# Performance work log

Hardware: AMD Instinct MI355X
Metric: run time of the kernel (lower is better)

The kernel has to match this reference:

```python
import jax, jax.numpy as jnp
import numpy as np

EPS = 1e-12
B, C, H, M, E, P = 2, 20000, 64, 8, 200000, 3


def setup_inputs() -> dict:
    key = jax.random.key(0)
    ks = jax.random.split(key, 24)
    inp = {}
    inp["features"] = jax.random.normal(ks[0], (B, C, H), jnp.float32)
    inp["positions"] = jax.random.normal(ks[1], (B, C, P), jnp.float32)
    inp["edge_index"] = jax.random.randint(ks[2], (2, E), 0, C)
    inp["degree"] = jax.random.randint(ks[3], (C,), 1, 33).astype(jnp.float32)
    inp["cell_node_indices"] = jax.random.randint(ks[4], (C, M), 0, C)
    mask = (jax.random.uniform(ks[5], (C, M)) > 0.3).astype(jnp.float32)
    inp["cell_node_mask"] = mask.at[:, 0].set(1.0)  # first node always valid (pad semantics)

    def lin(k, fan_in, fan_out):
        return (jax.random.normal(k, (fan_in, fan_out), jnp.float32) / np.sqrt(fan_in)).astype(jnp.float32)

    # message MLP: Linear(2H+4 -> H), SiLU, Linear(H -> H)
    inp["W1"] = lin(ks[6], 2 * H + 4, H); inp["b1"] = jnp.zeros((H,), jnp.float32)
    inp["W2"] = lin(ks[7], H, H);         inp["b2"] = jnp.zeros((H,), jnp.float32)
    # position MLP: Linear(H -> H), SiLU, Linear(H -> 1)
    inp["P1"] = lin(ks[8], H, H);  inp["pb1"] = jnp.zeros((H,), jnp.float32)
    inp["P2"] = lin(ks[9], H, 1);  inp["pb2"] = jnp.zeros((1,), jnp.float32)
    # update MLP: Linear(2H -> H), SiLU, Linear(H -> H)
    inp["U1"] = lin(ks[10], 2 * H, H); inp["ub1"] = jnp.zeros((H,), jnp.float32)
    inp["U2"] = lin(ks[11], H, H);     inp["ub2"] = jnp.zeros((H,), jnp.float32)
    return inp


def _mlp(x, Wa, ba, Wb, bb):
    return jax.nn.silu(x @ Wa + ba) @ Wb + bb


def _forward(features, positions, edge_index, degree, cell_node_indices, cell_node_mask,
             W1, b1, W2, b2, P1, pb1, P2, pb2, U1, ub1, U2, ub2):
    src, dst = edge_index[0], edge_index[1]
    # gather padded node positions per cell: [B, C, M, P]
    node_pos = positions[:, cell_node_indices]

    h_src = features[:, src]                      # [B,E,H]
    h_dst = features[:, dst]
    rel = positions[:, src] - positions[:, dst]   # [B,E,P]
    dist = jnp.linalg.norm(rel, axis=-1, keepdims=True)  # [B,E,1]

    sp = node_pos[:, src]                         # [B,E,M,P]
    dp = node_pos[:, dst]
    mx = cell_node_mask[src]                      # [E,M]
    my = cell_node_mask[dst]

    # pairwise distances [B,E,M,M] via gram trick (avoids [B,E,M,M,P] intermediate)
    sp2 = jnp.sum(sp * sp, -1)                    # [B,E,M]
    dp2 = jnp.sum(dp * dp, -1)
    cross = jnp.einsum('bemp,benp->bemn', sp, dp)
    d = jnp.sqrt(jnp.maximum(sp2[..., :, None] + dp2[..., None, :] - 2.0 * cross, 0.0) + EPS)

    # masked pairwise-distance sum
    w = mx[:, :, None] * my[:, None, :]           # [E,M,M]
    pairwise = jnp.sum(d * w[None], axis=(-1, -2))  # [B,E]

    # centroid distance
    denx = jnp.maximum(mx.sum(-1, keepdims=True), EPS)  # [E,1]
    deny = jnp.maximum(my.sum(-1, keepdims=True), EPS)
    cx = jnp.sum(sp * mx[None, :, :, None], axis=2) / denx[None]  # [B,E,P]
    cy = jnp.sum(dp * my[None, :, :, None], axis=2) / deny[None]
    centroid = jnp.linalg.norm(cx - cy, axis=-1)  # [B,E]

    # Hausdorff distance (masked min/max)
    inf = jnp.float32(jnp.inf)
    d_xy = jnp.where(my[None, :, None, :] <= 0, inf, d)
    min_xy = jnp.where(mx[None] <= 0, 0.0, d_xy.min(-1))  # [B,E,M]
    h_xy = min_xy.max(-1)                                  # [B,E]
    d_yx = jnp.where(mx[None, :, None, :] <= 0, inf, jnp.swapaxes(d, -1, -2))
    min_yx = jnp.where(my[None] <= 0, 0.0, d_yx.min(-1))
    h_yx = min_yx.max(-1)
    haus = jnp.maximum(h_xy, h_yx)

    invariants = jnp.concatenate([dist, pairwise[..., None], centroid[..., None], haus[..., None]], -1)  # [B,E,4]
    msg_in = jnp.concatenate([h_src, h_dst, invariants], -1)  # [B,E,2H+4]
    messages = _mlp(msg_in, W1, b1, W2, b2)                   # [B,E,H]

    # scatter-aggregate into destination cells, degree-normalize
    agg = jnp.zeros_like(features).at[:, dst].add(messages)
    agg = agg / jnp.maximum(degree, 1.0)[None, :, None]

    # position update
    wts = jnp.tanh(_mlp(messages, P1, pb1, P2, pb2))          # [B,E,1]
    pos_upd = jnp.zeros_like(positions).at[:, dst].add(wts * rel)

    new_features = features + _mlp(jnp.concatenate([features, agg], -1), U1, ub1, U2, ub2)
    new_positions = positions + pos_upd
    return new_features, new_positions


def reference(features, positions, edge_index, degree, cell_node_indices, cell_node_mask,
              W1, b1, W2, b2, P1, pb1, P2, pb2, U1, ub1, U2, ub2):
    return _forward(features, positions, edge_index, degree, cell_node_indices, cell_node_mask,
                    W1, b1, W2, b2, P1, pb1, P2, pb2, U1, ub1, U2, ub2)
```

## Files before the change

### kernel.cpp

```cpp
#include <hip/hip_runtime.h>
#include <hip/hip_bf16.h>

#define B_ 2
#define C_ 20000
#define H_ 64
#define M_ 8
#define E_ 200000
#define P_ 3
#define EPS_ 1e-12f
#define ET_ (E_ / 64)

typedef __attribute__((ext_vector_type(8))) short short8;
typedef __attribute__((ext_vector_type(4))) float float4v;

__device__ __forceinline__ float rcp_(float x)  { return __builtin_amdgcn_rcpf(x); }
__device__ __forceinline__ float sqrt_(float x) { return __builtin_amdgcn_sqrtf(x); }
__device__ __forceinline__ float silu_(float x) {
    return x * __builtin_amdgcn_rcpf(1.f + __expf(-x));
}
__device__ __forceinline__ float tanh_(float x) {
    float e = __expf(2.f * x);
    return 1.f - 2.f * __builtin_amdgcn_rcpf(e + 1.f);
}
__device__ __forceinline__ unsigned short f2b(float f) {
    unsigned u = __float_as_uint(f);
    unsigned r = (u + 0x7FFF + ((u >> 16) & 1)) >> 16;
    return (unsigned short)r;
}
__device__ __forceinline__ float b2f(unsigned short h) {
    return __uint_as_float(((unsigned)h) << 16);
}
__device__ __forceinline__ unsigned pk2u(float a, float b) {
    __hip_bfloat162 h = __float22bfloat162_rn(make_float2(a, b));
    unsigned u; __builtin_memcpy(&u, &h, sizeof(u)); return u;
}
__device__ __forceinline__ float lo16f(unsigned u) { return __uint_as_float(u << 16); }
__device__ __forceinline__ float hi16f(unsigned u) { return __uint_as_float(u & 0xFFFF0000u); }

#define W1S_OFF 0
#define W2S_OFF 8192
#define P1S_OFF 12288
#define U1S_OFF 16384
#define U2S_OFF 24576
#define WBUF_ELEMS 28672

#define NB_PREP  120
#define NB_FEATB 2500
#define NB_DESC  157
#define NB_HIST  782
#define NB_ZAGG  2500
#define NB_PCOPY 118
#define NB_COMBO (NB_PREP + NB_FEATB + NB_DESC + NB_HIST + NB_ZAGG + NB_PCOPY)


__global__ __launch_bounds__(256) void combo_kernel(
    const float* __restrict__ W1, const float* __restrict__ W2,
    const float* __restrict__ P1, const float* __restrict__ U1,
    const float* __restrict__ U2, unsigned short* __restrict__ wbuf,
    const float* __restrict__ feat, unsigned short* __restrict__ featb,
    const float* __restrict__ pos, const int* __restrict__ cni,
    const float* __restrict__ mask, unsigned* __restrict__ descp,
    const int* __restrict__ ei, int* __restrict__ cnt,
    float* __restrict__ aggf, float* __restrict__ out_pos)
{
    const int bid = blockIdx.x;
    if (bid < NB_PREP) {
        int t = bid * 256 + threadIdx.x;
        if (t >= WBUF_ELEMS) return;
        const float* W; int e;
        if (t < W2S_OFF)      { W = W1; e = t; }
        else if (t < U1S_OFF) { W = (t < P1S_OFF) ? W2 : P1; e = (t < P1S_OFF) ? t - W2S_OFF : t - P1S_OFF; }
        else if (t < U2S_OFF) { W = U1; e = t - U1S_OFF; }
        else                  { W = U2; e = t - U2S_OFF; }
        int j = e & 7, lane = (e >> 3) & 63, nt = (e >> 9) & 3, kk = e >> 11;
        int k = kk * 32 + ((lane >> 4) * 8) + j;
        int n = nt * 16 + (lane & 15);
        wbuf[t] = f2b(W[k * 64 + n]);
    } else if (bid < NB_PREP + NB_FEATB) {
        int t = (bid - NB_PREP) * 256 + threadIdx.x;
        float4 v = *(const float4*)&feat[(size_t)t * 4];
        *(uint2*)&featb[(size_t)t * 4] = make_uint2(pk2u(v.x, v.y), pk2u(v.z, v.w));
    } else if (bid < NB_PREP + NB_FEATB + NB_DESC) {
        int tid = (bid - NB_PREP - NB_FEATB) * 256 + threadIdx.x;
        if (tid >= B_ * C_) return;
        int b = tid / C_, c = tid - b * C_;
        const float* pb = pos + (size_t)b * C_ * P_;
        unsigned* D = descp + (size_t)tid * 32;
        int4 n0 = *(const int4*)&cni[c*8];
        int4 n1 = *(const int4*)&cni[c*8 + 4];
        float4 m0 = *(const float4*)&mask[c*8];
        float4 m1 = *(const float4*)&mask[c*8 + 4];
        int ni[8] = {n0.x, n0.y, n0.z, n0.w, n1.x, n1.y, n1.z, n1.w};
        float mm[8] = {m0.x, m0.y, m0.z, m0.w, m1.x, m1.y, m1.z, m1.w};
        float sx = 0.f, sy = 0.f, sz = 0.f, sm = 0.f;
        #pragma unroll
        for (int m = 0; m < 8; ++m) {
            float x = pb[ni[m]*3+0], y = pb[ni[m]*3+1], z = pb[ni[m]*3+2];
            ((uint2*)D)[m] = make_uint2(pk2u(x, y), pk2u(z, mm[m]));
            sx += x * mm[m]; sy += y * mm[m]; sz += z * mm[m]; sm += mm[m];
        }
        float inv = rcp_(fmaxf(sm, EPS_));
        *(float4*)(D + 16) = make_float4(sx * inv, sy * inv, sz * inv, sm);
        *(float4*)(D + 20) = make_float4(pb[c*3+0], pb[c*3+1], pb[c*3+2], 0.f);
    } else if (bid < NB_PREP + NB_FEATB + NB_DESC + NB_HIST) {
        int e = (bid - NB_PREP - NB_FEATB - NB_DESC) * 256 + threadIdx.x;
        if (e >= E_) return;
        atomicAdd(&cnt[ei[E_ + e]], 1);
    } else if (bid < NB_PREP + NB_FEATB + NB_DESC + NB_HIST + NB_ZAGG) {
        int t = (bid - NB_PREP - NB_FEATB - NB_DESC - NB_HIST) * 256 + threadIdx.x;
        *(float4*)&aggf[(size_t)t * 4] = make_float4(0.f, 0.f, 0.f, 0.f);
    } else {
        int t = (bid - NB_PREP - NB_FEATB - NB_DESC - NB_HIST - NB_ZAGG) * 256 + threadIdx.x;
        if (t >= (B_ * C_ * P_) / 4) return;
        *(float4*)&out_pos[(size_t)t * 4] = *(const float4*)&pos[(size_t)t * 4];
    }
}

__global__ __launch_bounds__(256) void alloc_kernel(
    const int* __restrict__ cnt, int* __restrict__ cursor, int* __restrict__ total)
{
    int idx = blockIdx.x * 256 + threadIdx.x;
    int lane = threadIdx.x & 63;
    int v = (idx < C_) ? cnt[idx] : 0;
    int inc = v;
    #pragma unroll
    for (int s = 1; s < 64; s <<= 1) {
        int n = __shfl_up(inc, s);
        if (lane >= s) inc += n;
    }
    int wtot = __shfl(inc, 63);
    int base = 0;
    if (lane == 0) base = atomicAdd(total, wtot);
    base = __shfl(base, 0);
    if (idx < C_) cursor[idx] = base + inc - v;
}

__global__ __launch_bounds__(256) void scatter_kernel(
    const int* __restrict__ ei, int* __restrict__ cursor, int2* __restrict__ sed)
{
    int e = blockIdx.x * 256 + threadIdx.x;
    if (e >= E_) return;
    int s = ei[e], d = ei[E_ + e];
    int slot = atomicAdd(&cursor[d], 1);
    sed[slot] = make_int2(s, d);
}

__global__ __launch_bounds__(256, 8) void edge_kernel(
    const unsigned short* __restrict__ featb,
    const int2* __restrict__ sed,
    const unsigned* __restrict__ descp,
    const unsigned short* __restrict__ wbuf, const float* __restrict__ W1,
    const float* __restrict__ b1, const float* __restrict__ b2,
    const float* __restrict__ pb1, const float* __restrict__ P2,
    const float* __restrict__ pb2,
    float* __restrict__ aggf, float* __restrict__ out_pos)
{
    __shared__ unsigned short lds[4 * 2304];

    const int tid  = threadIdx.x;
    const int w    = tid >> 6;
    const int lane = tid & 63;
    const int q    = lane >> 4;
    const int l16  = lane & 15;
    const int w16  = w * 16;

    const int bidr = blockIdx.x;
    const int xcd  = bidr & 7, kblk = bidr >> 3;
    const int qq   = (B_ * ET_) >> 3, rr_ = (B_ * ET_) & 7;
    const int tile = (xcd < rr_ ? xcd * (qq + 1) : rr_ * (qq + 1) + (xcd - rr_) * qq) + kblk;

    const int b    = tile / ET_;
    const int i0   = (tile - b * ET_) * 64;
    const unsigned short* fb = featb + (size_t)b * C_ * H_;

    const int2 sd  = sed[i0 + lane];
    const int s_l  = sd.x;
    const int d_l  = sd.y;
    const int sg   = __shfl(s_l, w16 + l16);
    const int dg   = __shfl(d_l, w16 + l16);

    unsigned short* Xw = lds + w * 2304;
    unsigned short* Hw = Xw;
    unsigned short* Mw = Xw + 1152;

    const unsigned* Ds = descp + ((size_t)b * C_ + sg) * 32;
    const unsigned* Dd = descp + ((size_t)b * C_ + dg) * 32;
    uint2 spk[8];
    #pragma unroll
    for (int i = 0; i < 8; ++i) spk[i] = ((const uint2*)Ds)[i];
    uint2 dpk[2];
    dpk[0] = ((const uint2*)Dd)[q*2 + 0];
    dpk[1] = ((const uint2*)Dd)[q*2 + 1];
    float4 Sc = *(const float4*)(Ds + 16), Dc = *(const float4*)(Dd + 16);
    float4 Sp = *(const float4*)(Ds + 20), Dp = *(const float4*)(Dd + 20);

    const float INFV = __builtin_inff();
    float4 S[8]; float rowmin[8];
    #pragma unroll
    for (int i = 0; i < 8; ++i) {
        S[i] = make_float4(lo16f(spk[i].x), hi16f(spk[i].x),
                           lo16f(spk[i].y), hi16f(spk[i].y));
        rowmin[i] = INFV;
    }
    float pair = 0.f, hyx = 0.f;
    #pragma unroll
    for (int jj = 0; jj < 2; ++jj) {
        float djx = lo16f(dpk[jj].x), djy = hi16f(dpk[jj].x);
        float djz = lo16f(dpk[jj].y), djw = hi16f(dpk[jj].y);
        float colmin = INFV;
        #pragma unroll
        for (int i = 0; i < 8; ++i) {
            float dx = S[i].x - djx, dy = S[i].y - djy, dz = S[i].z - djz;
            float dd = sqrt_(dx*dx + dy*dy + dz*dz + EPS_);
            pair += dd * S[i].w * djw;
            rowmin[i] = (djw    > 0.f) ? fminf(rowmin[i], dd) : rowmin[i];
            colmin    = (S[i].w > 0.f) ? fminf(colmin, dd)    : colmin;
        }
        hyx = fmaxf(hyx, (djw > 0.f) ? colmin : 0.f);
    }
    pair += __shfl_xor(pair, 16);  pair += __shfl_xor(pair, 32);
    hyx = fmaxf(hyx, __shfl_xor(hyx, 16));  hyx = fmaxf(hyx, __shfl_xor(hyx, 32));
    #pragma unroll
    for (int i = 0; i < 8; ++i) {
        rowmin[i] = fminf(rowmin[i], __shfl_xor(rowmin[i], 16));
        rowmin[i] = fminf(rowmin[i], __shfl_xor(rowmin[i], 32));
    }
    float hxy = 0.f;
    #pragma unroll
    for (int i = 0; i < 8; ++i)
        hxy = fmaxf(hxy, (S[i].w > 0.f) ? rowmin[i] : 0.f);
    float cdx = Sc.x - Dc.x, cdy = Sc.y - Dc.y, cdz = Sc.z - Dc.z;
    const float relx = Sp.x - Dp.x, rely = Sp.y - Dp.y, relz = Sp.z - Dp.z;
    const float ivx = sqrt_(relx*relx + rely*rely + relz*relz);
    const float ivy = pair;
    const float ivz = sqrt_(cdx*cdx + cdy*cdy + cdz*cdz);
    const float ivw = fmaxf(hxy, hyx);

    float4 iva[4];
    #pragma unroll
    for (int i = 0; i < 4; ++i) {
        int r = q*4 + i;
        iva[i] = make_float4(__shfl(ivx, r), __shfl(ivy, r),
                             __shfl(ivz, r), __shfl(ivw, r));
    }

    const int rr4 = lane >> 4, c4 = lane & 15;
    #pragma unroll
    for (int it = 0; it < 4; ++it) {
        int rloc = it * 4 + rr4;
        int r = w16 + rloc;
        int sr = __shfl(s_l, r);
        int dr = __shfl(d_l, r);
        uint2 vs = *(const uint2*)&fb[(size_t)sr * 64 + c4 * 4];
        uint2 vd = *(const uint2*)&fb[(size_t)dr * 64 + c4 * 4];
        *(uint2*)&Xw[rloc*136 + c4*4]      = vs;
        *(uint2*)&Xw[rloc*136 + 64 + c4*4] = vd;
    }

    float4v acc[4];
    #pragma unroll
    for (int nt = 0; nt < 4; ++nt) {
        float bv = b1[nt*16 + l16];
        float wa = W1[128*64 + nt*16 + l16];
        float wb = W1[129*64 + nt*16 + l16];
        float wc = W1[130*64 + nt*16 + l16];
        float wd = W1[131*64 + nt*16 + l16];
        #pragma unroll
        for (int i = 0; i < 4; ++i)
            acc[nt][i] = bv + iva[i].x*wa + iva[i].y*wb
                            + iva[i].z*wc + iva[i].w*wd;
    }
    #pragma unroll
    for (int kk = 0; kk < 4; ++kk) {
        short8 a = *(const short8*)&Xw[l16*136 + kk*32 + q*8];
        #pragma unroll
        for (int nt = 0; nt < 4; ++nt) {
            short8 bf = *(const short8*)&wbuf[W1S_OFF + (((kk*4 + nt)*64) + lane) * 8];
            acc[nt] = __builtin_amdgcn_mfma_f32_16x16x32_bf16(a, bf, acc[nt], 0, 0, 0);
        }
    }
    #pragma unroll
    for (int nt = 0; nt < 4; ++nt)
        #pragma unroll
        for (int i = 0; i < 4; i += 2) {
            unsigned u = pk2u(silu_(acc[nt][i]), silu_(acc[nt][i+1]));
            Hw[(q*4 + i)*72     + nt*16 + l16] = (unsigned short)u;
            Hw[(q*4 + i + 1)*72 + nt*16 + l16] = (unsigned short)(u >> 16);
        }

    float4v mac[4];
    #pragma unroll
    for (int nt = 0; nt < 4; ++nt) {
        float bv = b2[nt*16 + l16];
        mac[nt] = (float4v){bv, bv, bv, bv};
    }
    #pragma unroll
    for (int kk = 0; kk < 2; ++kk) {
        short8 a = *(const short8*)&Hw[l16*72 + kk*32 + q*8];
        #pragma unroll
        for (int nt = 0; nt < 4; ++nt) {
            short8 bf = *(const short8*)&wbuf[W2S_OFF + (((kk*4 + nt)*64) + lane) * 8];
            mac[nt] = __builtin_amdgcn_mfma_f32_16x16x32_bf16(a, bf, mac[nt], 0, 0, 0);
        }
    }
    #pragma unroll
    for (int nt = 0; nt < 4; ++nt)
        #pragma unroll
        for (int i = 0; i < 4; i += 2) {
            unsigned u = pk2u(mac[nt][i], mac[nt][i+1]);
            Mw[(q*4 + i)*72     + nt*16 + l16] = (unsigned short)u;
            Mw[(q*4 + i + 1)*72 + nt*16 + l16] = (unsigned short)(u >> 16);
        }

    float4v gac[4];
    #pragma unroll
    for (int nt = 0; nt < 4; ++nt) {
        float bv = pb1[nt*16 + l16];
        gac[nt] = (float4v){bv, bv, bv, bv};
    }
    #pragma unroll
    for (int kk = 0; kk < 2; ++kk) {
        short8 a = *(const short8*)&Mw[l16*72 + kk*32 + q*8];
        #pragma unroll
        for (int nt = 0; nt < 4; ++nt) {
            short8 bf = *(const short8*)&wbuf[P1S_OFF + (((kk*4 + nt)*64) + lane) * 8];
            gac[nt] = __builtin_amdgcn_mfma_f32_16x16x32_bf16(a, bf, gac[nt], 0, 0, 0);
        }
    }
    float p2v[4];
    #pragma unroll
    for (int nt = 0; nt < 4; ++nt) p2v[nt] = P2[nt*16 + l16];
    const float pb2v = pb2[0];

    #pragma unroll
    for (int i = 0; i < 4; ++i) {
        float p = 0.f;
        #pragma unroll
        for (int nt = 0; nt < 4; ++nt) p += silu_(gac[nt][i]) * p2v[nt];
        p += __shfl_xor(p, 8);
        p += __shfl_xor(p, 4);
        p += __shfl_xor(p, 2);
        p += __shfl_xor(p, 1);
        float wt = tanh_(p + pb2v);
        if (l16 == 0) *(float*)&Mw[(q*4 + i)*72 + 64] = wt;
    }

    float mrow[16];
    #pragma unroll
    for (int rr = 0; rr < 16; ++rr) mrow[rr] = b2f(Mw[rr*72 + lane]);
    float wtl = *(const float*)&Mw[l16*72 + 64];

    float* aggB = aggf + (size_t)b * C_ * 64;
    float* opB  = out_pos + (size_t)b * C_ * 3;

    int dnx = __shfl(d_l, (lane + 1) & 63);
    bool bf64 = (lane == 63) || (d_l != dnx);
    unsigned long long bm64t = __ballot(bf64) & 0x7FFFFFFFFFFFFFFFull;

    unsigned mask16 = (unsigned)((bm64t >> w16) & 0xFFFFull) | 0x8000u;
    const bool head_true = (w16 > 0) && ((bm64t >> (w16 - 1)) & 1ull);

    unsigned below = mask16 & ((1u << l16) - 1u);
    int dist = l16 - (below ? (31 - __clz((int)below)) : -1) - 1;

    {
        float sx = wtl * relx, sy = wtl * rely, sz = wtl * relz;
        #pragma unroll
        for (int s = 1; s < 16; s <<= 1) {
            float tx = __shfl_up(sx, s);
            float ty = __shfl_up(sy, s);
            float tz = __shfl_up(sz, s);
            if (dist >= s) { sx += tx; sy += ty; sz += tz; }
        }
        bool bflag = (mask16 >> l16) & 1u;
        if (bflag && q == 0) {
            float* p = &opB[(size_t)dg * 3];
            atomicAdd(p + 0, sx);
            atomicAdd(p + 1, sy);
            atomicAdd(p + 2, sz);
        }
    }

    float colacc = 0.f;
    int prev = -1;
    #pragma unroll
    for (int rr = 0; rr < 16; ++rr) {
        colacc += mrow[rr];
        if (mask16 & (1u << rr)) {
            int dseg = __builtin_amdgcn_readlane(dg, rr);
            bool tend   = (bm64t >> (w16 + rr)) & 1ull;
            bool tstart = (prev >= 0) || head_true;
            if (tend && tstart)
                aggB[(size_t)dseg * 64 + lane] = colacc;
            else
                atomicAdd(&aggB[(size_t)dseg * 64 + lane], colacc);
            colacc = 0.f;
            prev = rr;
        }
    }
}

__global__ __launch_bounds__(256, 8) void node_kernel(
    const unsigned short* __restrict__ featb,
    const float* __restrict__ aggf, const float* __restrict__ deg,
    const unsigned short* __restrict__ wbuf,
    const float* __restrict__ ub1, const float* __restrict__ ub2,
    float* __restrict__ out_feat)
{
    __shared__ unsigned short lds[4 * 2304];

    const int tid  = threadIdx.x;
    const int w    = tid >> 6;
    const int lane = tid & 63;
    const int q    = lane >> 4;
    const int l16  = lane & 15;
    const int g0   = blockIdx.x * 64;

    unsigned short* Xw = lds + w * 2304;
    unsigned short* Hw = Xw;

    const int rr4 = lane >> 4, c4 = lane & 15;
    #pragma unroll
    for (int it = 0; it < 4; ++it) {
        int rloc = it * 4 + rr4;
        int g = g0 + w*16 + rloc;
        int gc = (g >= C_) ? g - C_ : g;
        float sc = rcp_(fmaxf(deg[gc], 1.f));
        uint2  vf = *(const uint2*)&featb[(size_t)g * 64 + c4 * 4];
        float4 va = *(const float4*)&aggf[(size_t)g * 64 + c4 * 4];
        *(uint2*)&Xw[rloc*136 + c4*4]      = vf;
        *(uint2*)&Xw[rloc*136 + 64 + c4*4] =
            make_uint2(pk2u(va.x*sc, va.y*sc), pk2u(va.z*sc, va.w*sc));
    }

    float4v acc[4];
    #pragma unroll
    for (int nt = 0; nt < 4; ++nt) {
        float bv = ub1[nt*16 + l16];
        acc[nt] = (float4v){bv, bv, bv, bv};
    }
    #pragma unroll
    for (int kk = 0; kk < 4; ++kk) {
        short8 a = *(const short8*)&Xw[l16*136 + kk*32 + q*8];
        #pragma unroll
        for (int nt = 0; nt < 4; ++nt) {
            short8 bf = *(const short8*)&wbuf[U1S_OFF + (((kk*4 + nt)*64) + lane) * 8];
            acc[nt] = __builtin_amdgcn_mfma_f32_16x16x32_bf16(a, bf, acc[nt], 0, 0, 0);
        }
    }
    #pragma unroll
    for (int nt = 0; nt < 4; ++nt)
        #pragma unroll
        for (int i = 0; i < 4; i += 2) {
            unsigned u = pk2u(silu_(acc[nt][i]), silu_(acc[nt][i+1]));
            Hw[(q*4 + i)*72     + nt*16 + l16] = (unsigned short)u;
            Hw[(q*4 + i + 1)*72 + nt*16 + l16] = (unsigned short)(u >> 16);
        }

    float4v oac[4];
    #pragma unroll
    for (int nt = 0; nt < 4; ++nt) {
        float bv = ub2[nt*16 + l16];
        oac[nt] = (float4v){bv, bv, bv, bv};
    }
    #pragma unroll
    for (int kk = 0; kk < 2; ++kk) {
        short8 a = *(const short8*)&Hw[l16*72 + kk*32 + q*8];
        #pragma unroll
        for (int nt = 0; nt < 4; ++nt) {
            short8 bf = *(const short8*)&wbuf[U2S_OFF + (((kk*4 + nt)*64) + lane) * 8];
            oac[nt] = __builtin_amdgcn_mfma_f32_16x16x32_bf16(a, bf, oac[nt], 0, 0, 0);
        }
    }
    #pragma unroll
    for (int nt = 0; nt < 4; ++nt)
        #pragma unroll
        for (int i = 0; i < 4; ++i) {
            size_t idx = (size_t)(g0 + w*16 + q*4 + i) * 64 + nt*16 + l16;
            out_feat[idx] = b2f(featb[idx]) + oac[nt][i];
        }
}

extern "C" void kernel_launch(void* const* d_in, const int* in_sizes, int n_in,
                              void* d_out, int out_size, void* d_ws, size_t ws_size,
                              hipStream_t stream) {
    const float* feat = (const float*)d_in[0];
    const float* pos  = (const float*)d_in[1];
    const int*   ei   = (const int*)d_in[2];
    const float* deg  = (const float*)d_in[3];
    const int*   cni  = (const int*)d_in[4];
    const float* mask = (const float*)d_in[5];
    const float* W1   = (const float*)d_in[6];
    const float* b1   = (const float*)d_in[7];
    const float* W2   = (const float*)d_in[8];
    const float* b2   = (const float*)d_in[9];
    const float* P1   = (const float*)d_in[10];
    const float* pb1  = (const float*)d_in[11];
    const float* P2   = (const float*)d_in[12];
    const float* pb2  = (const float*)d_in[13];
    const float* U1   = (const float*)d_in[14];
    const float* ub1  = (const float*)d_in[15];
    const float* U2   = (const float*)d_in[16];
    const float* ub2  = (const float*)d_in[17];

    float* out_feat = (float*)d_out;
    float* out_pos  = out_feat + (size_t)B_ * C_ * H_;

    unsigned* descp = (unsigned*)d_ws;
    float*  aggf = (float*)(descp + (size_t)B_ * C_ * 32);
    unsigned short* featb = (unsigned short*)(aggf + (size_t)B_ * C_ * 64);
    unsigned short* wbuf  = featb + (size_t)B_ * C_ * 64;
    int* cnt    = (int*)(wbuf + WBUF_ELEMS);
    int* total  = cnt + C_;
    int* cursor = total + 1;
    int2* sed   = (int2*)(cursor + C_ + 1);

    hipMemsetAsync(cnt, 0, (C_ + 1) * sizeof(int), stream);

    combo_kernel<<<NB_COMBO, 256, 0, stream>>>(
        W1, W2, P1, U1, U2, wbuf, feat, featb, pos, cni, mask, descp, ei, cnt,
        aggf, out_pos);

    alloc_kernel<<<(C_ + 255) / 256, 256, 0, stream>>>(cnt, cursor, total);

    scatter_kernel<<<(E_ + 255) / 256, 256, 0, stream>>>(ei, cursor, sed);

    edge_kernel<<<B_ * ET_, 256, 0, stream>>>(
        featb, sed, descp, wbuf, W1, b1, b2, pb1, P2, pb2, aggf, out_pos);

    node_kernel<<<(B_ * C_) / 64, 256, 0, stream>>>(
        featb, aggf, deg, wbuf, ub1, ub2, out_feat);
}
```

Before: 211.6 us.

## Merge preprocessing, histogram, scan and scatter into one cooperative kernel

Replaces the memset, combo, alloc and scatter launches with a single cooperative kernel. It runs grid-stride phases separated by grid.sync: zeroing and layout prep, the dst histogram, the per-wave scan with atomic allocation, and the edge bucketing scatter. This removes several launch boundaries and the separate memset, at the cost of three grid-wide barriers and fewer resident blocks doing the elementwise work. It also relaxes the edge kernel's launch bounds from 8 to 6 waves per SIMD, which gives the compiler more registers but may lower occupancy.

Measured after the change: 572.5 us. 2.71x slower.

```diff
diff --git a/kernel.cpp b/kernel.cpp
--- a/kernel.cpp
+++ b/kernel.cpp
@@ -1,5 +1,8 @@
 #include <hip/hip_runtime.h>
 #include <hip/hip_bf16.h>
+#include <hip/hip_cooperative_groups.h>
+
+namespace cg = cooperative_groups;
 
 #define B_ 2
 #define C_ 20000
@@ -44,16 +47,10 @@
 #define U2S_OFF 24576
 #define WBUF_ELEMS 28672
 
-#define NB_PREP  120
-#define NB_FEATB 2500
-#define NB_DESC  157
-#define NB_HIST  782
-#define NB_ZAGG  2500
-#define NB_PCOPY 118
-#define NB_COMBO (NB_PREP + NB_FEATB + NB_DESC + NB_HIST + NB_ZAGG + NB_PCOPY)
-
-
-__global__ __launch_bounds__(256) void combo_kernel(
+
+#define PREP_NB 1024
+
+__global__ __launch_bounds__(256) void prep_kernel(
     const float* __restrict__ W1, const float* __restrict__ W2,
     const float* __restrict__ P1, const float* __restrict__ U1,
     const float* __restrict__ U2, unsigned short* __restrict__ wbuf,
@@ -61,31 +58,44 @@
     const float* __restrict__ pos, const int* __restrict__ cni,
     const float* __restrict__ mask, unsigned* __restrict__ descp,
     const int* __restrict__ ei, int* __restrict__ cnt,
-    float* __restrict__ aggf, float* __restrict__ out_pos)
+    int* __restrict__ cursor, int* __restrict__ total,
+    float* __restrict__ aggf, float* __restrict__ out_pos,
+    int2* __restrict__ sed)
 {
-    const int bid = blockIdx.x;
-    if (bid < NB_PREP) {
-        int t = bid * 256 + threadIdx.x;
-        if (t >= WBUF_ELEMS) return;
+    cg::grid_group grid = cg::this_grid();
+    const int gtid = blockIdx.x * 256 + threadIdx.x;
+    const int nthr = PREP_NB * 256;
+    const int lane = threadIdx.x & 63;
+
+    for (int t = gtid; t <= C_; t += nthr) cnt[t] = 0;
+
+    for (int t = gtid; t < WBUF_ELEMS; t += nthr) {
         const float* W; int e;
         if (t < W2S_OFF)      { W = W1; e = t; }
         else if (t < U1S_OFF) { W = (t < P1S_OFF) ? W2 : P1; e = (t < P1S_OFF) ? t - W2S_OFF : t - P1S_OFF; }
         else if (t < U2S_OFF) { W = U1; e = t - U1S_OFF; }
         else                  { W = U2; e = t - U2S_OFF; }
-        int j = e & 7, lane = (e >> 3) & 63, nt = (e >> 9) & 3, kk = e >> 11;
-        int k = kk * 32 + ((lane >> 4) * 8) + j;
-        int n = nt * 16 + (lane & 15);
+        int j = e & 7, ln = (e >> 3) & 63, nt = (e >> 9) & 3, kk = e >> 11;
+        int k = kk * 32 + ((ln >> 4) * 8) + j;
+        int n = nt * 16 + (ln & 15);
         wbuf[t] = f2b(W[k * 64 + n]);
-    } else if (bid < NB_PREP + NB_FEATB) {
-        int t = (bid - NB_PREP) * 256 + threadIdx.x;
+    }
+
+    for (int t = gtid; t < (B_ * C_ * H_) / 4; t += nthr) {
         float4 v = *(const float4*)&feat[(size_t)t * 4];
         *(uint2*)&featb[(size_t)t * 4] = make_uint2(pk2u(v.x, v.y), pk2u(v.z, v.w));
-    } else if (bid < NB_PREP + NB_FEATB + NB_DESC) {
-        int tid = (bid - NB_PREP - NB_FEATB) * 256 + threadIdx.x;
-        if (tid >= B_ * C_) return;
-        int b = tid / C_, c = tid - b * C_;
+    }
+
+    for (int t = gtid; t < (B_ * C_ * H_) / 4; t += nthr)
+        *(float4*)&aggf[(size_t)t * 4] = make_float4(0.f, 0.f, 0.f, 0.f);
+
+    for (int t = gtid; t < (B_ * C_ * P_) / 4; t += nthr)
+        *(float4*)&out_pos[(size_t)t * 4] = *(const float4*)&pos[(size_t)t * 4];
+
+    for (int t = gtid; t < B_ * C_; t += nthr) {
+        int b = t / C_, c = t - b * C_;
         const float* pb = pos + (size_t)b * C_ * P_;
-        unsigned* D = descp + (size_t)tid * 32;
+        unsigned* D = descp + (size_t)t * 32;
         int4 n0 = *(const int4*)&cni[c*8];
         int4 n1 = *(const int4*)&cni[c*8 + 4];
         float4 m0 = *(const float4*)&mask[c*8];
@@ -102,50 +112,43 @@
         float inv = rcp_(fmaxf(sm, EPS_));
         *(float4*)(D + 16) = make_float4(sx * inv, sy * inv, sz * inv, sm);
         *(float4*)(D + 20) = make_float4(pb[c*3+0], pb[c*3+1], pb[c*3+2], 0.f);
-    } else if (bid < NB_PREP + NB_FEATB + NB_DESC + NB_HIST) {
-        int e = (bid - NB_PREP - NB_FEATB - NB_DESC) * 256 + threadIdx.x;
-        if (e >= E_) return;
+    }
+
+    grid.sync();
+
+    for (int e = gtid; e < E_; e += nthr)
         atomicAdd(&cnt[ei[E_ + e]], 1);
-    } else if (bid < NB_PREP + NB_FEATB + NB_DESC + NB_HIST + NB_ZAGG) {
-        int t = (bid - NB_PREP - NB_FEATB - NB_DESC - NB_HIST) * 256 + threadIdx.x;
-        *(float4*)&aggf[(size_t)t * 4] = make_float4(0.f, 0.f, 0.f, 0.f);
-    } else {
-        int t = (bid - NB_PREP - NB_FEATB - NB_DESC - NB_HIST - NB_ZAGG) * 256 + threadIdx.x;
-        if (t >= (B_ * C_ * P_) / 4) return;
-        *(float4*)&out_pos[(size_t)t * 4] = *(const float4*)&pos[(size_t)t * 4];
-    }
-}
-
-__global__ __launch_bounds__(256) void alloc_kernel(
-    const int* __restrict__ cnt, int* __restrict__ cursor, int* __restrict__ total)
-{
-    int idx = blockIdx.x * 256 + threadIdx.x;
-    int lane = threadIdx.x & 63;
-    int v = (idx < C_) ? cnt[idx] : 0;
-    int inc = v;
-    #pragma unroll
-    for (int s = 1; s < 64; s <<= 1) {
-        int n = __shfl_up(inc, s);
-        if (lane >= s) inc += n;
-    }
-    int wtot = __shfl(inc, 63);
-    int base = 0;
-    if (lane == 0) base = atomicAdd(total, wtot);
-    base = __shfl(base, 0);
-    if (idx < C_) cursor[idx] = base + inc - v;
-}
-
-__global__ __launch_bounds__(256) void scatter_kernel(
-    const int* __restrict__ ei, int* __restrict__ cursor, int2* __restrict__ sed)
-{
-    int e = blockIdx.x * 256 + threadIdx.x;
-    if (e >= E_) return;
-    int s = ei[e], d = ei[E_ + e];
-    int slot = atomicAdd(&cursor[d], 1);
-    sed[slot] = make_int2(s, d);
-}
-
-__global__ __launch_bounds__(256, 8) void edge_kernel(
+
+    grid.sync();
+
+    {
+        int idx = gtid;
+        if (idx - lane < C_) {
+            int v = (idx < C_) ? cnt[idx] : 0;
+            int inc = v;
+            #pragma unroll
+            for (int s = 1; s < 64; s <<= 1) {
+                int n = __shfl_up(inc, s);
+                if (lane >= s) inc += n;
+            }
+            int wtot = __shfl(inc, 63);
+            int base = 0;
+            if (lane == 0) base = atomicAdd(total, wtot);
+            base = __shfl(base, 0);
+            if (idx < C_) cursor[idx] = base + inc - v;
+        }
+    }
+
+    grid.sync();
+
+    for (int e = gtid; e < E_; e += nthr) {
+        int s = ei[e], d = ei[E_ + e];
+        int slot = atomicAdd(&cursor[d], 1);
+        sed[slot] = make_int2(s, d);
+    }
+}
+
+__global__ __launch_bounds__(256, 6) void edge_kernel(
     const unsigned short* __restrict__ featb,
     const int2* __restrict__ sed,
     const unsigned* __restrict__ descp,
@@ -515,15 +518,17 @@
     int* cursor = total + 1;
     int2* sed   = (int2*)(cursor + C_ + 1);
 
-    hipMemsetAsync(cnt, 0, (C_ + 1) * sizeof(int), stream);
-
-    combo_kernel<<<NB_COMBO, 256, 0, stream>>>(
-        W1, W2, P1, U1, U2, wbuf, feat, featb, pos, cni, mask, descp, ei, cnt,
-        aggf, out_pos);
-
-    alloc_kernel<<<(C_ + 255) / 256, 256, 0, stream>>>(cnt, cursor, total);
-
-    scatter_kernel<<<(E_ + 255) / 256, 256, 0, stream>>>(ei, cursor, sed);
+    {
+        void* args[] = {
+            (void*)&W1, (void*)&W2, (void*)&P1, (void*)&U1, (void*)&U2,
+            (void*)&wbuf, (void*)&feat, (void*)&featb, (void*)&pos,
+            (void*)&cni, (void*)&mask, (void*)&descp, (void*)&ei,
+            (void*)&cnt, (void*)&cursor, (void*)&total,
+            (void*)&aggf, (void*)&out_pos, (void*)&sed
+        };
+        hipLaunchCooperativeKernel((const void*)prep_kernel,
+                                   dim3(PREP_NB), dim3(256), args, 0, stream);
+    }
 
     edge_kernel<<<B_ * ET_, 256, 0, stream>>>(
         featb, sed, descp, wbuf, W1, b1, b2, pb1, P2, pb2, aggf, out_pos);
```
